# Kernel tuning notes

Measured on AMD Instinct MI355X. Metric: run time of the kernel, lower is better.

Reference implementation:

```python
import jax, jax.numpy as jnp
import numpy as np

H = 20  # GRU hidden size (fixed in the module)


def gru_cell(x, h, Wih, Whh, bih, bhh):
    # PyTorch GRU cell math. x: (B, F), h: (B, H)
    gi = x @ Wih.T + bih  # (B, 3H)
    gh = h @ Whh.T + bhh  # (B, 3H)
    i_r, i_z, i_n = jnp.split(gi, 3, axis=-1)
    h_r, h_z, h_n = jnp.split(gh, 3, axis=-1)
    r = jax.nn.sigmoid(i_r + h_r)
    z = jax.nn.sigmoid(i_z + h_z)
    n = jnp.tanh(i_n + r * h_n)
    return (1.0 - z) * n + z * h


def setup_inputs() -> dict:
    key = jax.random.key(0)
    ks = jax.random.split(key, 16)
    B, S, R = 1024, 1024, 12
    F = R + 4 + 4 + 8 + 8  # 36 = input_record_width + embedding output_dim
    x = jax.random.normal(ks[0], (B, S, R), dtype=jnp.float32)
    onehots = jax.random.randint(ks[1], (B, S, 4), 0, 10, dtype=jnp.int64)
    s = 0.1
    inp = {
        'x': x, 'onehots': onehots,
        'emb0': jax.random.normal(ks[2], (10, 4), jnp.float32) * s,
        'emb1': jax.random.normal(ks[3], (20, 4), jnp.float32) * s,
        'emb2': jax.random.normal(ks[4], (50, 8), jnp.float32) * s,
        'emb3': jax.random.normal(ks[5], (100, 8), jnp.float32) * s,
        'Wih1': jax.random.normal(ks[6], (3 * H, F), jnp.float32) * s,
        'Whh1': jax.random.normal(ks[7], (3 * H, H), jnp.float32) * s,
        'bih1': jax.random.normal(ks[8], (3 * H,), jnp.float32) * s,
        'bhh1': jax.random.normal(ks[9], (3 * H,), jnp.float32) * s,
        'Wih2': jax.random.normal(ks[10], (3 * H, F), jnp.float32) * s,
        'Whh2': jax.random.normal(ks[11], (3 * H, H), jnp.float32) * s,
        'bih2': jax.random.normal(ks[12], (3 * H,), jnp.float32) * s,
        'bhh2': jax.random.normal(ks[13], (3 * H,), jnp.float32) * s,
        'Wfc': jax.random.normal(ks[14], (F, H), jnp.float32) * s,
        'bfc': jax.random.normal(ks[15], (F,), jnp.float32) * s,
    }
    return inp


def reference(x, onehots, emb0, emb1, emb2, emb3,
              Wih1, Whh1, bih1, bhh1, Wih2, Whh2, bih2, bhh2, Wfc, bfc):
    # Onehot embedding: lookup per categorical column, concat
    emb = jnp.concatenate([
        emb0[onehots[..., 0]], emb1[onehots[..., 1]],
        emb2[onehots[..., 2]], emb3[onehots[..., 3]],
    ], axis=-1)
    xin = jnp.concatenate([x, emb], axis=-1)  # (B, S, F)
    origin = xin
    B, S, F = xin.shape

    # Encoder GRU (gru1) over the sequence; keep only final hidden state
    h0 = jnp.zeros((B, H), xin.dtype)

    def enc_step(h, xt):
        return gru_cell(xt, h, Wih1, Whh1, bih1, bhh1), None

    h_last, _ = jax.lax.scan(enc_step, h0, jnp.swapaxes(xin, 0, 1))
    h = jnp.tanh(h_last)
    x0 = jnp.tanh(h @ Wfc.T + bfc)  # first decoded step

    def dec_step(carry, _):
        xprev, hprev = carry
        hnew = jnp.tanh(gru_cell(xprev, hprev, Wih2, Whh2, bih2, bhh2))
        xnew = jnp.tanh(hnew @ Wfc.T + bfc)
        return (xnew, hnew), xnew

    _, rest = jax.lax.scan(dec_step, (x0, h), None, length=S - 1)  # (S-1, B, F)
    xs = jnp.concatenate([x0[None], rest], axis=0)  # (S, B, F)
    xs = jnp.swapaxes(xs, 0, 1)[:, ::-1]  # (B, S, F), flipped along time
    return (origin, xs)
```

## Files before the change

### kernel.cpp

```cpp
#include <hip/hip_runtime.h>

#define BATCH 1024
#define SEQ   1024
#define FDIM  36
#define HID   20
#define G3    60
#define CR    64
#define NCHUNK (SEQ/CR)

typedef float v2f __attribute__((ext_vector_type(2)));

__device__ __forceinline__ float fast_sigmoid(float x){
    return __builtin_amdgcn_rcpf(1.0f + __expf(-x));
}
__device__ __forceinline__ float fast_tanh(float x){
    return fmaf(-2.0f, __builtin_amdgcn_rcpf(1.0f + __expf(2.0f*x)), 1.0f);
}

#define READLANE_F(v, u) __int_as_float(__builtin_amdgcn_readlane(__float_as_int(v), (u)))

__global__ __launch_bounds__(128, 2)
void gru_fused(const float* __restrict__ x,
               const int* __restrict__ oh,
               const float* __restrict__ e0, const float* __restrict__ e1,
               const float* __restrict__ e2, const float* __restrict__ e3,
               const float* __restrict__ Wih1g, const float* __restrict__ Whh1g,
               const float* __restrict__ bih1g, const float* __restrict__ bhh1g,
               const float* __restrict__ Wih2g, const float* __restrict__ Whh2g,
               const float* __restrict__ bih2g, const float* __restrict__ bhh2g,
               const float* __restrict__ Wfcg,  const float* __restrict__ bfcg,
               float* __restrict__ origin, float* __restrict__ out2)
{
    __shared__ __align__(16) float gbuf[2][CR][G3];
    __shared__ __align__(16) float psh[64];
    __shared__ __align__(16) float dsh[64];

    const int lane   = threadIdx.x & 63;
    const bool is_enc = (threadIdx.x < 64);
    const int b = __builtin_amdgcn_readfirstlane(blockIdx.x);

    const int k = lane < G3 ? lane : G3 - 1;

    float whh1[HID];
    float bh1 = 0.f;
    float hs[HID];
    float hv = 0.0f;
    if (is_enc) {
        #pragma unroll
        for (int u = 0; u < HID; u++) whh1[u] = Whh1g[k * HID + u];
        bh1 = bhh1g[k];
        #pragma unroll
        for (int u = 0; u < HID; u++) hs[u] = 0.0f;
    }

    const int j = lane;
    const float* tbl; int ohc, eshift, sub;
    if (j < 16)      { tbl = e0; ohc = 0; eshift = 2; sub = j - 12; }
    else if (j < 20) { tbl = e1; ohc = 1; eshift = 2; sub = j - 16; }
    else if (j < 28) { tbl = e2; ohc = 2; eshift = 3; sub = j - 20; }
    else             { tbl = e3; ohc = 3; eshift = 3; sub = j - 28; }
    if (sub < 0) sub = 0;
    if (sub > 7) sub = 7;
    const bool from_x = (j < 12);
    const float* pa = from_x ? (x + j) : (tbl + sub);
    v2f w1p[FDIM/2]; float bi1 = 0.f;
    if (!is_enc) {
        #pragma unroll
        for (int q = 0; q < FDIM/2; q++) w1p[q] = ((const v2f*)(Wih1g + k * FDIM))[q];
        bi1 = bih1g[k];
    }

#define GATE_STEP(GIV, WHH, BH, HVAR) do {                                   \
        float h0 = BH, h1 = 0.f, h2 = 0.f, h3 = 0.f;                         \
        _Pragma("unroll")                                                    \
        for (int uu = 0; uu < HID; uu += 4) {                                \
            h0 = fmaf(WHH[uu + 0], hs[uu + 0], h0);                          \
            h1 = fmaf(WHH[uu + 1], hs[uu + 1], h1);                          \
            h2 = fmaf(WHH[uu + 2], hs[uu + 2], h2);                          \
            h3 = fmaf(WHH[uu + 3], hs[uu + 3], h3);                          \
        }                                                                    \
        float gh = (h0 + h1) + (h2 + h3);                                    \
        float v   = (GIV) + gh;                                              \
        float vz  = __shfl(v,    (lane + 20) & 63);                          \
        float in_ = __shfl((GIV),(lane + 40) & 63);                          \
        float hn  = __shfl(gh,   (lane + 40) & 63);                          \
        float r = fast_sigmoid(v);                                           \
        float z = fast_sigmoid(vz);                                          \
        float n = fast_tanh(fmaf(r, hn, in_));                               \
        HVAR = n + z * (HVAR - n);                                           \
        _Pragma("unroll")                                                    \
        for (int uu = 0; uu < HID; uu++) hs[uu] = READLANE_F(HVAR, uu);      \
    } while (0)

#define CONSUME_CHUNK(CB) do {                                               \
        const float* gp = &gbuf[CB][0][k];                                   \
        float ga = gp[0], gbv = gp[G3];                                      \
        _Pragma("unroll 1")                                                  \
        for (int i = 0; i < CR; i += 2) {                                    \
            float ge = ga, go = gbv;                                         \
            if (i < CR - 2) ga = gp[(i + 2) * G3];                           \
            GATE_STEP(ge, whh1, bh1, hv);                                    \
            if (i < CR - 2) gbv = gp[(i + 3) * G3];                          \
            GATE_STEP(go, whh1, bh1, hv);                                    \
        }                                                                    \
    } while (0)

    #pragma unroll 1
    for (int c = 0; c < NCHUNK; ++c) {
        if (!is_enc) {
            const int rbase = b * SEQ + c * CR;
            float* gdst = &gbuf[c & 1][0][0];
            const float4* xp4 = (const float4*)psh;
            #pragma unroll 1
            for (int g = 0; g < CR / 8; ++g) {
                int ohv[8];
                #pragma unroll
                for (int n = 0; n < 8; n++)
                    ohv[n] = oh[(rbase + 8 * g + n) * 4 + ohc];
                float valv[8];
                #pragma unroll
                for (int n = 0; n < 8; n++) {
                    int R = rbase + 8 * g + n;
                    int off = from_x ? (R * 12) : (ohv[n] << eshift);
                    valv[n] = pa[off];
                }
                #pragma unroll
                for (int n = 0; n < 8; n++) {
                    const int i = 8 * g + n;
                    const size_t R = (size_t)(rbase + i);
                    psh[lane] = valv[n];
                    if (lane < FDIM) origin[R * FDIM + lane] = valv[n];
                    v2f a0 = {bi1, 0.f}, a1 = {0.f, 0.f};
                    #pragma unroll
                    for (int q = 0; q < 9; q++) {
                        float4 xv4 = xp4[q];
                        v2f xlo = {xv4.x, xv4.y}, xhi = {xv4.z, xv4.w};
                        a0 = __builtin_elementwise_fma(w1p[2*q],     xlo, a0);
                        a1 = __builtin_elementwise_fma(w1p[2*q + 1], xhi, a1);
                    }
                    float gg = (a0.x + a1.x) + (a0.y + a1.y);
                    if (lane < G3) gdst[i * G3 + lane] = gg;
                }
            }
        } else if (c > 0) {
            CONSUME_CHUNK((c - 1) & 1);
        }
        __syncthreads();
    }
    if (!is_enc) return;

    CONSUME_CHUNK((NCHUNK - 1) & 1);

    const int kf = lane < FDIM ? lane : FDIM - 1;
    float whh2[HID], wfc[HID];
    v2f wih2p[FDIM/2];
    #pragma unroll
    for (int q = 0; q < FDIM/2; q++) wih2p[q] = ((const v2f*)(Wih2g + k * FDIM))[q];
    #pragma unroll
    for (int u = 0; u < HID; u++) whh2[u] = Whh2g[k * HID + u];
    #pragma unroll
    for (int u = 0; u < HID; u++) wfc[u] = Wfcg[kf * HID + u];
    const float bi2 = bih2g[k], bh2 = bhh2g[k];
    const float bf  = bfcg[kf];

    float hvd = fast_tanh(hv);
    #pragma unroll
    for (int u = 0; u < HID; u++) hs[u] = READLANE_F(hvd, u);

    float* orow = out2 + ((size_t)b * SEQ + (SEQ - 1)) * FDIM;

    float xv;
    {
        float a0 = bf, a1 = 0.f, a2 = 0.f, a3 = 0.f;
        #pragma unroll
        for (int u = 0; u < HID; u += 4) {
            a0 = fmaf(wfc[u + 0], hs[u + 0], a0);
            a1 = fmaf(wfc[u + 1], hs[u + 1], a1);
            a2 = fmaf(wfc[u + 2], hs[u + 2], a2);
            a3 = fmaf(wfc[u + 3], hs[u + 3], a3);
        }
        xv = fast_tanh((a0 + a1) + (a2 + a3));
    }
    dsh[lane] = xv;
    if (lane < FDIM) orow[lane] = xv;

    const v2f* xp = (const v2f*)dsh;
    #pragma unroll 1
    for (int d = 1; d < SEQ; ++d) {
        orow -= FDIM;
        v2f xs2[FDIM/2];
        #pragma unroll
        for (int q = 0; q < FDIM/2; q++) xs2[q] = xp[q];
        float h0 = bh2, h1 = 0.f, h2 = 0.f, h3 = 0.f;
        #pragma unroll
        for (int u = 0; u < HID; u += 4) {
            h0 = fmaf(whh2[u + 0], hs[u + 0], h0);
            h1 = fmaf(whh2[u + 1], hs[u + 1], h1);
            h2 = fmaf(whh2[u + 2], hs[u + 2], h2);
            h3 = fmaf(whh2[u + 3], hs[u + 3], h3);
        }
        float gh = (h0 + h1) + (h2 + h3);
        v2f accA = {bi2, 0.f}, accB = {0.f, 0.f};
        #pragma unroll
        for (int q = 0; q < FDIM/2; q += 2) {
            accA = __builtin_elementwise_fma(wih2p[q],     xs2[q],     accA);
            accB = __builtin_elementwise_fma(wih2p[q + 1], xs2[q + 1], accB);
        }
        float gi = (accA.x + accB.x) + (accA.y + accB.y);
        float v   = gi + gh;
        float vz  = __shfl(v,  (lane + 20) & 63);
        float in_ = __shfl(gi, (lane + 40) & 63);
        float hn  = __shfl(gh, (lane + 40) & 63);
        float r = fast_sigmoid(v);
        float z = fast_sigmoid(vz);
        float n = fast_tanh(fmaf(r, hn, in_));
        float hraw = n + z * (hvd - n);
        hvd = fast_tanh(hraw);
        #pragma unroll
        for (int u = 0; u < HID; u++) hs[u] = READLANE_F(hvd, u);
        float a0 = bf, a1 = 0.f, a2 = 0.f, a3 = 0.f;
        #pragma unroll
        for (int u = 0; u < HID; u += 4) {
            a0 = fmaf(wfc[u + 0], hs[u + 0], a0);
            a1 = fmaf(wfc[u + 1], hs[u + 1], a1);
            a2 = fmaf(wfc[u + 2], hs[u + 2], a2);
            a3 = fmaf(wfc[u + 3], hs[u + 3], a3);
        }
        xv = fast_tanh((a0 + a1) + (a2 + a3));
        dsh[lane] = xv;
        if (lane < FDIM) orow[lane] = xv;
    }
}

extern "C" void kernel_launch(void* const* d_in, const int* in_sizes, int n_in,
                              void* d_out, int out_size, void* d_ws, size_t ws_size,
                              hipStream_t stream) {
    const float* x    = (const float*)d_in[0];
    const int*   oh   = (const int*)d_in[1];
    const float* e0   = (const float*)d_in[2];
    const float* e1   = (const float*)d_in[3];
    const float* e2   = (const float*)d_in[4];
    const float* e3   = (const float*)d_in[5];
    const float* Wih1 = (const float*)d_in[6];
    const float* Whh1 = (const float*)d_in[7];
    const float* bih1 = (const float*)d_in[8];
    const float* bhh1 = (const float*)d_in[9];
    const float* Wih2 = (const float*)d_in[10];
    const float* Whh2 = (const float*)d_in[11];
    const float* bih2 = (const float*)d_in[12];
    const float* bhh2 = (const float*)d_in[13];
    const float* Wfc  = (const float*)d_in[14];
    const float* bfc  = (const float*)d_in[15];

    float* out    = (float*)d_out;
    float* origin = out;
    float* out2   = out + (size_t)BATCH * SEQ * FDIM;

    gru_fused<<<BATCH, 128, 0, stream>>>(x, oh, e0, e1, e2, e3,
                                         Wih1, Whh1, bih1, bhh1,
                                         Wih2, Whh2, bih2, bhh2,
                                         Wfc, bfc, origin, out2);
}
```

Before: 984.6 us.

## Remap GRU gate lanes to compute two gates per lane and drop cross-lane shuffles

Lanes are remapped so each lane computes two gate pre-activations: lanes 0-31 compute r and n, lanes 32-63 compute z. This replaces three ds_bpermute shuffles per step with one permlane32 swap in both the encoder and the decoder recurrences. The decoder now broadcasts the input vector with readlane instead of going through LDS, removing an LDS round trip per step. The encoder producer prefetches one-hot indices and values a group ahead. It doubles per-lane FMA work and raises register pressure (two weight rows plus the full Wih2 rows), and it relies on permlane32_swap being available on gfx950.

```diff
diff --git a/kernel.cpp b/kernel.cpp
--- a/kernel.cpp
+++ b/kernel.cpp
@@ -9,6 +9,7 @@
 #define NCHUNK (SEQ/CR)
 
 typedef float v2f __attribute__((ext_vector_type(2)));
+typedef int   v2i __attribute__((ext_vector_type(2)));
 
 __device__ __forceinline__ float fast_sigmoid(float x){
     return __builtin_amdgcn_rcpf(1.0f + __expf(-x));
@@ -18,6 +19,17 @@
 }
 
 #define READLANE_F(v, u) __int_as_float(__builtin_amdgcn_readlane(__float_as_int(v), (u)))
+
+__device__ __forceinline__ float upper_half_of(float s){
+#if __has_builtin(__builtin_amdgcn_permlane32_swap)
+    v2i pr = __builtin_amdgcn_permlane32_swap(__float_as_int(s), __float_as_int(s), false, false);
+    return (__int_as_float(pr.x) + __int_as_float(pr.y)) - s;
+#else
+    float a = s, b = s;
+    asm("v_permlane32_swap_b32 %0, %1" : "+v"(a), "+v"(b));
+    return (a + b) - s;
+#endif
+}
 
 __global__ __launch_bounds__(128, 2)
 void gru_fused(const float* __restrict__ x,
@@ -33,26 +45,32 @@
 {
     __shared__ __align__(16) float gbuf[2][CR][G3];
     __shared__ __align__(16) float psh[64];
-    __shared__ __align__(16) float dsh[64];
 
     const int lane   = threadIdx.x & 63;
     const bool is_enc = (threadIdx.x < 64);
     const int b = __builtin_amdgcn_readfirstlane(blockIdx.x);
 
-    const int k = lane < G3 ? lane : G3 - 1;
-
-    float whh1[HID];
-    float bh1 = 0.f;
+    const int ulr = lane & 31;
+    const int ul  = ulr < HID ? ulr : HID - 1;
+    const int kA  = (lane < 32) ? ul : (HID + ul);
+    const int kB  = (lane < 32) ? (2 * HID + ul) : (HID + ul);
+
+    float whh1A[HID], whh1B[HID];
+    float bh1A = 0.f, bh1B = 0.f;
     float hs[HID];
     float hv = 0.0f;
     if (is_enc) {
         #pragma unroll
-        for (int u = 0; u < HID; u++) whh1[u] = Whh1g[k * HID + u];
-        bh1 = bhh1g[k];
+        for (int u = 0; u < HID; u++) whh1A[u] = Whh1g[kA * HID + u];
+        #pragma unroll
+        for (int u = 0; u < HID; u++) whh1B[u] = Whh1g[kB * HID + u];
+        bh1A = bhh1g[kA];
+        bh1B = bhh1g[kB];
         #pragma unroll
         for (int u = 0; u < HID; u++) hs[u] = 0.0f;
     }
 
+    const int k = lane < G3 ? lane : G3 - 1;
     const int j = lane;
     const float* tbl; int ohc, eshift, sub;
     if (j < 16)      { tbl = e0; ohc = 0; eshift = 2; sub = j - 12; }
@@ -70,38 +88,42 @@
         bi1 = bih1g[k];
     }
 
-#define GATE_STEP(GIV, WHH, BH, HVAR) do {                                   \
-        float h0 = BH, h1 = 0.f, h2 = 0.f, h3 = 0.f;                         \
+#define GATE_STEP2(GIA, GIB, WA, WB, BA, BB, HVAR) do {                      \
+        float a0 = (BA), a1 = 0.f, a2 = 0.f, a3 = 0.f;                       \
+        float b0 = (BB), b1 = 0.f, b2 = 0.f, b3 = 0.f;                       \
         _Pragma("unroll")                                                    \
         for (int uu = 0; uu < HID; uu += 4) {                                \
-            h0 = fmaf(WHH[uu + 0], hs[uu + 0], h0);                          \
-            h1 = fmaf(WHH[uu + 1], hs[uu + 1], h1);                          \
-            h2 = fmaf(WHH[uu + 2], hs[uu + 2], h2);                          \
-            h3 = fmaf(WHH[uu + 3], hs[uu + 3], h3);                          \
+            a0 = fmaf(WA[uu + 0], hs[uu + 0], a0);                           \
+            a1 = fmaf(WA[uu + 1], hs[uu + 1], a1);                           \
+            a2 = fmaf(WA[uu + 2], hs[uu + 2], a2);                           \
+            a3 = fmaf(WA[uu + 3], hs[uu + 3], a3);                           \
+            b0 = fmaf(WB[uu + 0], hs[uu + 0], b0);                           \
+            b1 = fmaf(WB[uu + 1], hs[uu + 1], b1);                           \
+            b2 = fmaf(WB[uu + 2], hs[uu + 2], b2);                           \
+            b3 = fmaf(WB[uu + 3], hs[uu + 3], b3);                           \
         }                                                                    \
-        float gh = (h0 + h1) + (h2 + h3);                                    \
-        float v   = (GIV) + gh;                                              \
-        float vz  = __shfl(v,    (lane + 20) & 63);                          \
-        float in_ = __shfl((GIV),(lane + 40) & 63);                          \
-        float hn  = __shfl(gh,   (lane + 40) & 63);                          \
-        float r = fast_sigmoid(v);                                           \
-        float z = fast_sigmoid(vz);                                          \
-        float n = fast_tanh(fmaf(r, hn, in_));                               \
-        HVAR = n + z * (HVAR - n);                                           \
+        float ghA = (a0 + a1) + (a2 + a3);                                   \
+        float ghB = (b0 + b1) + (b2 + b3);                                   \
+        float s_  = fast_sigmoid((GIA) + ghA);        \
+        float z_  = upper_half_of(s_);                \
+        float n_  = fast_tanh(fmaf(s_, ghB, (GIB)));                         \
+        HVAR = n_ + z_ * (HVAR - n_);                                        \
         _Pragma("unroll")                                                    \
         for (int uu = 0; uu < HID; uu++) hs[uu] = READLANE_F(HVAR, uu);      \
     } while (0)
 
-#define CONSUME_CHUNK(CB) do {                                               \
-        const float* gp = &gbuf[CB][0][k];                                   \
-        float ga = gp[0], gbv = gp[G3];                                      \
+#define CONSUME_CHUNK2(CB) do {                                              \
+        const float* gpA = &gbuf[CB][0][0] + kA;                             \
+        const float* gpB = &gbuf[CB][0][0] + kB;                             \
+        float gA0 = gpA[0],  gB0 = gpB[0];                                   \
+        float gA1 = gpA[G3], gB1 = gpB[G3];                                  \
         _Pragma("unroll 1")                                                  \
         for (int i = 0; i < CR; i += 2) {                                    \
-            float ge = ga, go = gbv;                                         \
-            if (i < CR - 2) ga = gp[(i + 2) * G3];                           \
-            GATE_STEP(ge, whh1, bh1, hv);                                    \
-            if (i < CR - 2) gbv = gp[(i + 3) * G3];                          \
-            GATE_STEP(go, whh1, bh1, hv);                                    \
+            float eA = gA0, eB = gB0, oA = gA1, oB = gB1;                    \
+            if (i < CR - 2) { gA0 = gpA[(i + 2) * G3]; gB0 = gpB[(i + 2) * G3]; } \
+            GATE_STEP2(eA, eB, whh1A, whh1B, bh1A, bh1B, hv);                \
+            if (i < CR - 2) { gA1 = gpA[(i + 3) * G3]; gB1 = gpB[(i + 3) * G3]; } \
+            GATE_STEP2(oA, oB, whh1A, whh1B, bh1A, bh1B, hv);                \
         }                                                                    \
     } while (0)
 
@@ -111,25 +133,39 @@
             const int rbase = b * SEQ + c * CR;
             float* gdst = &gbuf[c & 1][0][0];
             const float4* xp4 = (const float4*)psh;
+            int ohA[8], ohB[8]; float valA[8];
+            #pragma unroll
+            for (int n = 0; n < 8; n++) ohA[n] = oh[(rbase + n) * 4 + ohc];
+            #pragma unroll
+            for (int n = 0; n < 8; n++) ohB[n] = oh[(rbase + 8 + n) * 4 + ohc];
+            #pragma unroll
+            for (int n = 0; n < 8; n++) {
+                int R = rbase + n;
+                int off = from_x ? (R * 12) : (ohA[n] << eshift);
+                valA[n] = pa[off];
+            }
             #pragma unroll 1
             for (int g = 0; g < CR / 8; ++g) {
-                int ohv[8];
-                #pragma unroll
-                for (int n = 0; n < 8; n++)
-                    ohv[n] = oh[(rbase + 8 * g + n) * 4 + ohc];
-                float valv[8];
-                #pragma unroll
-                for (int n = 0; n < 8; n++) {
-                    int R = rbase + 8 * g + n;
-                    int off = from_x ? (R * 12) : (ohv[n] << eshift);
-                    valv[n] = pa[off];
+                int ohN[8]; float valB[8];
+                if (g < 6) {
+                    #pragma unroll
+                    for (int n = 0; n < 8; n++)
+                        ohN[n] = oh[(rbase + 8 * (g + 2) + n) * 4 + ohc];
+                }
+                if (g < 7) {
+                    #pragma unroll
+                    for (int n = 0; n < 8; n++) {
+                        int R = rbase + 8 * (g + 1) + n;
+                        int off = from_x ? (R * 12) : (ohB[n] << eshift);
+                        valB[n] = pa[off];
+                    }
                 }
                 #pragma unroll
                 for (int n = 0; n < 8; n++) {
                     const int i = 8 * g + n;
                     const size_t R = (size_t)(rbase + i);
-                    psh[lane] = valv[n];
-                    if (lane < FDIM) origin[R * FDIM + lane] = valv[n];
+                    psh[lane] = valA[n];
+                    if (lane < FDIM) origin[R * FDIM + lane] = valA[n];
                     v2f a0 = {bi1, 0.f}, a1 = {0.f, 0.f};
                     #pragma unroll
                     for (int q = 0; q < 9; q++) {
@@ -141,27 +177,40 @@
                     float gg = (a0.x + a1.x) + (a0.y + a1.y);
                     if (lane < G3) gdst[i * G3 + lane] = gg;
                 }
+                if (g < 6) {
+                    #pragma unroll
+                    for (int n = 0; n < 8; n++) ohB[n] = ohN[n];
+                }
+                if (g < 7) {
+                    #pragma unroll
+                    for (int n = 0; n < 8; n++) valA[n] = valB[n];
+                }
             }
         } else if (c > 0) {
-            CONSUME_CHUNK((c - 1) & 1);
+            CONSUME_CHUNK2((c - 1) & 1);
         }
         __syncthreads();
     }
     if (!is_enc) return;
 
-    CONSUME_CHUNK((NCHUNK - 1) & 1);
+    CONSUME_CHUNK2((NCHUNK - 1) & 1);
 
     const int kf = lane < FDIM ? lane : FDIM - 1;
-    float whh2[HID], wfc[HID];
-    v2f wih2p[FDIM/2];
-    #pragma unroll
-    for (int q = 0; q < FDIM/2; q++) wih2p[q] = ((const v2f*)(Wih2g + k * FDIM))[q];
-    #pragma unroll
-    for (int u = 0; u < HID; u++) whh2[u] = Whh2g[k * HID + u];
+    float wihA[FDIM], wihB[FDIM];
+    float whh2A[HID], whh2B[HID], wfc[HID];
+    #pragma unroll
+    for (int q = 0; q < FDIM; q++) wihA[q] = Wih2g[kA * FDIM + q];
+    #pragma unroll
+    for (int q = 0; q < FDIM; q++) wihB[q] = Wih2g[kB * FDIM + q];
+    #pragma unroll
+    for (int u = 0; u < HID; u++) whh2A[u] = Whh2g[kA * HID + u];
+    #pragma unroll
+    for (int u = 0; u < HID; u++) whh2B[u] = Whh2g[kB * HID + u];
     #pragma unroll
     for (int u = 0; u < HID; u++) wfc[u] = Wfcg[kf * HID + u];
-    const float bi2 = bih2g[k], bh2 = bhh2g[k];
-    const float bf  = bfcg[kf];
+    const float biA  = bih2g[kA], biB  = bih2g[kB];
+    const float bh2A = bhh2g[kA], bh2B = bhh2g[kB];
+    const float bf   = bfcg[kf];
 
     float hvd = fast_tanh(hv);
     #pragma unroll
@@ -171,63 +220,73 @@
 
     float xv;
     {
-        float a0 = bf, a1 = 0.f, a2 = 0.f, a3 = 0.f;
+        float f0 = bf, f1 = 0.f, f2 = 0.f, f3 = 0.f;
         #pragma unroll
         for (int u = 0; u < HID; u += 4) {
-            a0 = fmaf(wfc[u + 0], hs[u + 0], a0);
-            a1 = fmaf(wfc[u + 1], hs[u + 1], a1);
-            a2 = fmaf(wfc[u + 2], hs[u + 2], a2);
-            a3 = fmaf(wfc[u + 3], hs[u + 3], a3);
-        }
-        xv = fast_tanh((a0 + a1) + (a2 + a3));
-    }
-    dsh[lane] = xv;
+            f0 = fmaf(wfc[u + 0], hs[u + 0], f0);
+            f1 = fmaf(wfc[u + 1], hs[u + 1], f1);
+            f2 = fmaf(wfc[u + 2], hs[u + 2], f2);
+            f3 = fmaf(wfc[u + 3], hs[u + 3], f3);
+        }
+        xv = fast_tanh((f0 + f1) + (f2 + f3));
+    }
     if (lane < FDIM) orow[lane] = xv;
 
-    const v2f* xp = (const v2f*)dsh;
     #pragma unroll 1
     for (int d = 1; d < SEQ; ++d) {
         orow -= FDIM;
-        v2f xs2[FDIM/2];
-        #pragma unroll
-        for (int q = 0; q < FDIM/2; q++) xs2[q] = xp[q];
-        float h0 = bh2, h1 = 0.f, h2 = 0.f, h3 = 0.f;
+        float c0 = biA, c1 = 0.f, c2 = 0.f, c3 = 0.f, c4 = 0.f, c5 = 0.f;
+        float e0_ = biB, e1_ = 0.f, e2_ = 0.f, e3_ = 0.f, e4_ = 0.f, e5_ = 0.f;
+        #pragma unroll
+        for (int q = 0; q < FDIM; q += 6) {
+            float x0_ = READLANE_F(xv, q + 0);
+            float x1_ = READLANE_F(xv, q + 1);
+            float x2_ = READLANE_F(xv, q + 2);
+            float x3_ = READLANE_F(xv, q + 3);
+            float x4_ = READLANE_F(xv, q + 4);
+            float x5_ = READLANE_F(xv, q + 5);
+            c0  = fmaf(wihA[q + 0], x0_, c0);   e0_ = fmaf(wihB[q + 0], x0_, e0_);
+            c1  = fmaf(wihA[q + 1], x1_, c1);   e1_ = fmaf(wihB[q + 1], x1_, e1_);
+            c2  = fmaf(wihA[q + 2], x2_, c2);   e2_ = fmaf(wihB[q + 2], x2_, e2_);
+            c3  = fmaf(wihA[q + 3], x3_, c3);   e3_ = fmaf(wihB[q + 3], x3_, e3_);
+            c4  = fmaf(wihA[q + 4], x4_, c4);   e4_ = fmaf(wihB[q + 4], x4_, e4_);
+            c5  = fmaf(wihA[q + 5], x5_, c5);   e5_ = fmaf(wihB[q + 5], x5_, e5_);
+        }
+        float giA = ((c0 + c1) + (c2 + c3)) + (c4 + c5);
+        float giB = ((e0_ + e1_) + (e2_ + e3_)) + (e4_ + e5_);
+
+        float a0 = bh2A, a1 = 0.f, a2 = 0.f, a3 = 0.f;
+        float b0 = bh2B, b1 = 0.f, b2 = 0.f, b3 = 0.f;
         #pragma unroll
         for (int u = 0; u < HID; u += 4) {
-            h0 = fmaf(whh2[u + 0], hs[u + 0], h0);
-            h1 = fmaf(whh2[u + 1], hs[u + 1], h1);
-            h2 = fmaf(whh2[u + 2], hs[u + 2], h2);
-            h3 = fmaf(whh2[u + 3], hs[u + 3], h3);
-        }
-        float gh = (h0 + h1) + (h2 + h3);
-        v2f accA = {bi2, 0.f}, accB = {0.f, 0.f};
-        #pragma unroll
-        for (int q = 0; q < FDIM/2; q += 2) {
-            accA = __builtin_elementwise_fma(wih2p[q],     xs2[q],     accA);
-            accB = __builtin_elementwise_fma(wih2p[q + 1], xs2[q + 1], accB);
-        }
-        float gi = (accA.x + accB.x) + (accA.y + accB.y);
-        float v   = gi + gh;
-        float vz  = __shfl(v,  (lane + 20) & 63);
-        float in_ = __shfl(gi, (lane + 40) & 63);
-        float hn  = __shfl(gh, (lane + 40) & 63);
-        float r = fast_sigmoid(v);
-        float z = fast_sigmoid(vz);
-        float n = fast_tanh(fmaf(r, hn, in_));
-        float hraw = n + z * (hvd - n);
-        hvd = fast_tanh(hraw);
+            a0 = fmaf(whh2A[u + 0], hs[u + 0], a0);
+            a1 = fmaf(whh2A[u + 1], hs[u + 1], a1);
+            a2 = fmaf(whh2A[u + 2], hs[u + 2], a2);
+            a3 = fmaf(whh2A[u + 3], hs[u + 3], a3);
+            b0 = fmaf(whh2B[u + 0], hs[u + 0], b0);
+            b1 = fmaf(whh2B[u + 1], hs[u + 1], b1);
+            b2 = fmaf(whh2B[u + 2], hs[u + 2], b2);
+            b3 = fmaf(whh2B[u + 3], hs[u + 3], b3);
+        }
+        float ghA = (a0 + a1) + (a2 + a3);
+        float ghB = (b0 + b1) + (b2 + b3);
+
+        float s_ = fast_sigmoid(giA + ghA);
+        float z_ = upper_half_of(s_);
+        float n_ = fast_tanh(fmaf(s_, ghB, giB));
+        hvd = fast_tanh(fmaf(z_, hvd - n_, n_));
         #pragma unroll
         for (int u = 0; u < HID; u++) hs[u] = READLANE_F(hvd, u);
-        float a0 = bf, a1 = 0.f, a2 = 0.f, a3 = 0.f;
+
+        float f0 = bf, f1 = 0.f, f2 = 0.f, f3 = 0.f;
         #pragma unroll
         for (int u = 0; u < HID; u += 4) {
-            a0 = fmaf(wfc[u + 0], hs[u + 0], a0);
-            a1 = fmaf(wfc[u + 1], hs[u + 1], a1);
-            a2 = fmaf(wfc[u + 2], hs[u + 2], a2);
-            a3 = fmaf(wfc[u + 3], hs[u + 3], a3);
-        }
-        xv = fast_tanh((a0 + a1) + (a2 + a3));
-        dsh[lane] = xv;
+            f0 = fmaf(wfc[u + 0], hs[u + 0], f0);
+            f1 = fmaf(wfc[u + 1], hs[u + 1], f1);
+            f2 = fmaf(wfc[u + 2], hs[u + 2], f2);
+            f3 = fmaf(wfc[u + 3], hs[u + 3], f3);
+        }
+        xv = fast_tanh((f0 + f1) + (f2 + f3));
         if (lane < FDIM) orow[lane] = xv;
     }
 }
```

Result: slower. 1.453 ms (+47.6%).
